# Optimization experiments

Measured on AMD Instinct MI355X. Metric: run time of the kernel, lower is better.

Reference implementation:

```python
import jax, jax.numpy as jnp
import numpy as np

EPS = 1e-6
K = 20  # n_knn from init


def _vnt_weight(W):
    # VNT linear: rows normalized to sum to 1 (which_norm_VNT='norm') for translation equivariance
    return W / jnp.sum(W, axis=1, keepdims=True)


def _lin(W, x):
    # apply [out,in] weight over channel axis 1 of x: [B, C_in, 3, ...] -> [B, C_out, 3, ...]
    return jnp.einsum('oi,bi...->bo...', W, x)


def _vn_lrelu(x, Wf, Wd, vnt=False):
    # VN(T)LinearLeakyReLU with negative_slope=0.0, no batchnorm. Vector axis is axis 2.
    Wp = _vnt_weight(Wf) if vnt else Wf
    p = _lin(Wp, x)
    d = _lin(Wd, x)
    dot = jnp.sum(p * d, axis=2, keepdims=True)
    dsq = jnp.sum(d * d, axis=2, keepdims=True)
    return jnp.where(dot >= 0, p, p - (dot / (dsq + EPS)) * d)


def _knn(pts, k):
    # pts: [B,N,3] -> indices of k nearest (self included), via -||xi-xj||^2 top_k
    sq = jnp.sum(pts * pts, axis=-1)                      # [B,N]
    inner = jnp.einsum('bnd,bmd->bnm', pts, pts)          # [B,N,N]
    neg_dist = 2.0 * inner - sq[:, :, None] - sq[:, None, :]
    return jax.lax.top_k(neg_dist, k)[1]                  # [B,N,k]


def _graph_feature_cross(x, k):
    # x: [B,3,N] -> edge features [B, 3(feat: nbr-ctr, ctr, cross), 3(vec), N, k]
    pts = jnp.transpose(x, (0, 2, 1))                     # [B,N,3]
    idx = _knn(pts, k)                                    # [B,N,k]
    nbr = jax.vmap(lambda p, i: p[i])(pts, idx)           # [B,N,k,3]
    ctr = jnp.broadcast_to(pts[:, :, None, :], nbr.shape)
    cross = jnp.cross(nbr, ctr)
    feat = jnp.stack([nbr - ctr, ctr, cross], axis=3)     # [B,N,k,3feat,3vec]
    return jnp.transpose(feat, (0, 3, 4, 1, 2))           # [B,3feat,3vec,N,k]


def _forward(x, Wpos_f, Wpos_d, Wc1_f, Wc1_d, Wc2_f, Wc2_d, Wt_f, Wt_d, W1_f, W1_d, W2_f, W2_d, W3):
    feat = _graph_feature_cross(x, K)                     # [B,3,3,N,K]
    h = _vn_lrelu(feat, Wpos_f, Wpos_d, vnt=True)         # [B,64,3,N,K]
    h = h.mean(axis=-1)                                   # mean pool over k -> [B,64,3,N]
    x2 = _vn_lrelu(h, Wc1_f, Wc1_d, vnt=True)             # conv_center_
    xc = _vn_lrelu(x2, Wc2_f, Wc2_d, vnt=True)            # conv_center
    tx = _vn_lrelu(xc, Wt_f, Wt_d, vnt=True)              # conv_trans [B,12,3,N]
    trans_latent = tx.mean(axis=-1)                       # [B,12,3]
    h = h - xc                                            # center features
    h = _vn_lrelu(h, W1_f, W1_d)                          # conv1
    h = _vn_lrelu(h, W2_f, W2_d)                          # conv2
    h = _lin(W3, h)                                       # conv3 (plain VNLinear) [B,116,3,N]
    rot_latent = h.mean(axis=-1)                          # [B,116,3]
    return jnp.concatenate([rot_latent, trans_latent], axis=1)  # [B,128,3]


def setup_inputs() -> dict:
    key = jax.random.key(0)
    ks = jax.random.split(key, 16)
    B, N, C = 4, 4096, 64
    ROT = 116  # c_dim - trans_c_dim

    def w(k, o, i):
        return jax.random.normal(k, (o, i), jnp.float32) * 0.1

    def wt(k, o, i):
        # VNT weights: row sums kept near 1 so normalization is well-conditioned
        return jax.random.normal(k, (o, i), jnp.float32) * 0.02 + 1.0 / i

    return {
        'x': jax.random.normal(ks[0], (B, 3, N), jnp.float32),
        'Wpos_f': wt(ks[1], C, 3), 'Wpos_d': w(ks[2], C, 3),
        'Wc1_f': wt(ks[3], C, C), 'Wc1_d': w(ks[4], C, C),
        'Wc2_f': wt(ks[5], C, C), 'Wc2_d': w(ks[6], C, C),
        'Wt_f': wt(ks[7], 12, C), 'Wt_d': w(ks[8], 12, C),
        'W1_f': w(ks[9], C, C), 'W1_d': w(ks[10], C, C),
        'W2_f': w(ks[11], C, C), 'W2_d': w(ks[12], C, C),
        'W3': w(ks[13], ROT, C),
    }


def reference(x, Wpos_f, Wpos_d, Wc1_f, Wc1_d, Wc2_f, Wc2_d, Wt_f, Wt_d, W1_f, W1_d, W2_f, W2_d, W3):
    return _forward(x, Wpos_f, Wpos_d, Wc1_f, Wc1_d, Wc2_f, Wc2_d, Wt_f, Wt_d, W1_f, W1_d, W2_f, W2_d, W3)
```

## Files before the change

### kernel.cpp

```cpp
#include <hip/hip_runtime.h>

#define NPTS 4096
#define BATCH 4
#define KNN 20
#define ROT 116

__device__ __forceinline__ void vn_lrelu3(float p[3], const float d[3]) {
  float dot = p[0]*d[0] + p[1]*d[1] + p[2]*d[2];
  if (dot < 0.0f) {
    float dsq = d[0]*d[0] + d[1]*d[1] + d[2]*d[2];
    float r = dot / (dsq + 1e-6f);
    p[0] -= r*d[0]; p[1] -= r*d[1]; p[2] -= r*d[2];
  }
}

__global__ __launch_bounds__(256) void knn_edge_kernel(const float* __restrict__ x,
                                                       const float* __restrict__ Wf,
                                                       const float* __restrict__ Wd,
                                                       float* __restrict__ h) {
  const int row = blockIdx.x;
  const int b = row >> 12, i = row & (NPTS - 1);
  const float* __restrict__ xb = x + b * 3 * NPTS;
  const float cx = xb[i], cy = xb[NPTS + i], cz = xb[2 * NPTS + i];
  const int t = threadIdx.x;
  const int j0 = t << 4;

  __shared__ unsigned int hist[2048];
  __shared__ unsigned int ld_[384];
  __shared__ int lj_[384];
  __shared__ unsigned int lcount;
  __shared__ int s_B;
  __shared__ int wtot[4];
  __shared__ int s_nbr[KNN];
  __shared__ float e[KNN][3][3];
  __shared__ float part[4][64][3];

  for (int k = t; k < 2048; k += 256) hist[k] = 0u;
  if (t == 0) lcount = 0u;
  __syncthreads();

  unsigned int db[16];
#pragma unroll
  for (int q = 0; q < 4; ++q) {
    const float4 px = *(const float4*)(xb + j0 + 4 * q);
    const float4 py = *(const float4*)(xb + NPTS + j0 + 4 * q);
    const float4 pz = *(const float4*)(xb + 2 * NPTS + j0 + 4 * q);
    float dx, dy, dz, dd;
    dx = px.x - cx; dy = py.x - cy; dz = pz.x - cz;
    dd = dx*dx + dy*dy + dz*dz; db[4*q+0] = __float_as_uint(dd);
    dx = px.y - cx; dy = py.y - cy; dz = pz.y - cz;
    dd = dx*dx + dy*dy + dz*dz; db[4*q+1] = __float_as_uint(dd);
    dx = px.z - cx; dy = py.z - cy; dz = pz.z - cz;
    dd = dx*dx + dy*dy + dz*dz; db[4*q+2] = __float_as_uint(dd);
    dx = px.w - cx; dy = py.w - cy; dz = pz.w - cz;
    dd = dx*dx + dy*dy + dz*dz; db[4*q+3] = __float_as_uint(dd);
  }
#pragma unroll
  for (int s = 0; s < 16; ++s) atomicAdd(&hist[db[s] >> 20], 1u);
  __syncthreads();

  int v = 0;
#pragma unroll
  for (int s = 0; s < 8; ++s) v += (int)hist[t * 8 + s];
  const int myps = v;
  const int lane = t & 63;
#pragma unroll
  for (int off = 1; off < 64; off <<= 1) {
    int n = __shfl_up(v, off);
    if (lane >= off) v += n;
  }
  if (lane == 63) wtot[t >> 6] = v;
  __syncthreads();
  int woff = 0;
#pragma unroll
  for (int w = 0; w < 4; ++w) if (w < (t >> 6)) woff += wtot[w];
  const int cum_in = v + woff;
  const int cum_ex = cum_in - myps;
  if (cum_ex < KNN && cum_in >= KNN) {
    int cum = cum_ex, B = t * 8;
    for (int s = 0; s < 8; ++s) {
      const int hh = (int)hist[t * 8 + s];
      if (cum + hh >= KNN) { B = t * 8 + s; break; }
      cum += hh;
    }
    s_B = B;
  }
  __syncthreads();
  const unsigned int Bb = (unsigned int)s_B;
#pragma unroll
  for (int s = 0; s < 16; ++s) {
    if ((db[s] >> 20) <= Bb) {
      unsigned int pos = atomicAdd(&lcount, 1u);
      if (pos < 384u) { ld_[pos] = db[s]; lj_[pos] = j0 + s; }
    }
  }
  __syncthreads();
  const int n = min((int)lcount, 384);
  for (int idx = t; idx < n; idx += 256) {
    const unsigned int kd = ld_[idx]; const int kj = lj_[idx];
    int rank = 0;
    for (int m = 0; m < n; ++m) {
      const unsigned int md = ld_[m];
      rank += (md < kd || (md == kd && lj_[m] < kj)) ? 1 : 0;
    }
    if (rank < KNN) s_nbr[rank] = kj;
  }
  __syncthreads();

  if (t < KNN) {
    const int j = s_nbr[t];
    const float nx = xb[j], ny = xb[NPTS + j], nz = xb[2 * NPTS + j];
    e[t][0][0] = nx - cx; e[t][0][1] = ny - cy; e[t][0][2] = nz - cz;
    e[t][1][0] = cx;      e[t][1][1] = cy;      e[t][1][2] = cz;
    e[t][2][0] = ny * cz - nz * cy;
    e[t][2][1] = nz * cx - nx * cz;
    e[t][2][2] = nx * cy - ny * cx;
  }
  __syncthreads();

  const int c = t & 63, kg = t >> 6;
  float f0 = Wf[c * 3 + 0], f1 = Wf[c * 3 + 1], f2 = Wf[c * 3 + 2];
  const float s = 1.0f / (f0 + f1 + f2);
  f0 *= s; f1 *= s; f2 *= s;
  const float d0 = Wd[c * 3 + 0], d1 = Wd[c * 3 + 1], d2 = Wd[c * 3 + 2];
  float a0 = 0.f, a1 = 0.f, a2 = 0.f;
#pragma unroll
  for (int kk = 0; kk < 5; ++kk) {
    const int k = kg * 5 + kk;
    float pv[3], dv[3];
#pragma unroll
    for (int vv = 0; vv < 3; ++vv) {
      pv[vv] = f0 * e[k][0][vv] + f1 * e[k][1][vv] + f2 * e[k][2][vv];
      dv[vv] = d0 * e[k][0][vv] + d1 * e[k][1][vv] + d2 * e[k][2][vv];
    }
    vn_lrelu3(pv, dv);
    a0 += pv[0]; a1 += pv[1]; a2 += pv[2];
  }
  part[kg][c][0] = a0; part[kg][c][1] = a1; part[kg][c][2] = a2;
  __syncthreads();
  if (t < 64) {
    const float inv = 1.0f / KNN;
    float* hp = h + (size_t)row * 192 + t * 3;
#pragma unroll
    for (int vv = 0; vv < 3; ++vv)
      hp[vv] = (part[0][t][vv] + part[1][t][vv] + part[2][t][vv] + part[3][t][vv]) * inv;
  }
}

template<bool VNT, int MODE>
__global__ __launch_bounds__(256) void layer_batch(
    const float* in, float* out, float* aux,
    const float* __restrict__ Wf, const float* __restrict__ Wd) {
  __shared__ float wfT[64][65], wdT[64][65];
  __shared__ float act[4][4][64][4];
  const int t = threadIdx.x, q = t >> 6, c = t & 63;
  for (int e = t; e < 4096; e += 256) {
    wfT[e & 63][e >> 6] = Wf[e];
    wdT[e & 63][e >> 6] = Wd[e];
  }
  __syncthreads();
  if (VNT) {
    if (t < 64) {
      float s = 0.f;
      for (int i = 0; i < 64; ++i) s += wfT[i][t];
      s = 1.0f / s;
      for (int i = 0; i < 64; ++i) wfT[i][t] *= s;
    }
    __syncthreads();
  }
  const int pbase = (blockIdx.x * 4 + q) * 8;
  float r0 = 0.f, r1 = 0.f, r2 = 0.f;
  for (int pass = 0; pass < 2; ++pass) {
    const int p0 = pbase + pass * 4;
#pragma unroll
    for (int p = 0; p < 4; ++p) {
      const float* ip = in + (size_t)(p0 + p) * 192 + c * 3;
      *(float4*)act[q][p][c] = make_float4(ip[0], ip[1], ip[2], 0.f);
    }
    __builtin_amdgcn_wave_barrier();
    float af[12], ad[12];
#pragma unroll
    for (int e = 0; e < 12; ++e) { af[e] = 0.f; ad[e] = 0.f; }
    for (int i = 0; i < 64; ++i) {
      const float wfv = wfT[i][c];
      const float wdv = wdT[i][c];
#pragma unroll
      for (int p = 0; p < 4; ++p) {
        const float4 hv = *(const float4*)act[q][p][i];
        af[p*3+0] += wfv * hv.x; af[p*3+1] += wfv * hv.y; af[p*3+2] += wfv * hv.z;
        ad[p*3+0] += wdv * hv.x; ad[p*3+1] += wdv * hv.y; ad[p*3+2] += wdv * hv.z;
      }
    }
    __builtin_amdgcn_wave_barrier();
#pragma unroll
    for (int p = 0; p < 4; ++p) {
      float pf[3] = { af[p*3+0], af[p*3+1], af[p*3+2] };
      float pd[3] = { ad[p*3+0], ad[p*3+1], ad[p*3+2] };
      vn_lrelu3(pf, pd);
      const size_t ofs = (size_t)(p0 + p) * 192 + c * 3;
      if (MODE == 0) {
        out[ofs+0] = pf[0]; out[ofs+1] = pf[1]; out[ofs+2] = pf[2];
      } else if (MODE == 1) {
        const float h0 = aux[ofs+0], h1 = aux[ofs+1], h2 = aux[ofs+2];
        aux[ofs+0] = h0 - pf[0]; aux[ofs+1] = h1 - pf[1]; aux[ofs+2] = h2 - pf[2];
        out[ofs+0] = pf[0]; out[ofs+1] = pf[1]; out[ofs+2] = pf[2];
      } else {
        r0 += pf[0]; r1 += pf[1]; r2 += pf[2];
      }
    }
    __builtin_amdgcn_wave_barrier();
  }
  if (MODE == 2) {
    *(float4*)act[q][0][c] = make_float4(r0, r1, r2, 0.f);
    __syncthreads();
    if (t < 192) {
      const int cc = t / 3, vv = t - cc * 3;
      out[blockIdx.x * 192 + t] =
          act[0][0][cc][vv] + act[1][0][cc][vv] + act[2][0][cc][vv] + act[3][0][cc][vv];
    }
  }
}

__global__ __launch_bounds__(256) void trans_kernel(
    const float* __restrict__ xc,
    const float* __restrict__ Wtf, const float* __restrict__ Wtd,
    float* __restrict__ trans_part) {
  __shared__ float wtf[12][65], wtd[12][65];
  __shared__ float xpt[4][64][4];
  __shared__ float tred[4][12][3];
  const int t = threadIdx.x, q = t >> 6, l = t & 63;
  for (int e = t; e < 768; e += 256) {
    wtf[e >> 6][e & 63] = Wtf[e]; wtd[e >> 6][e & 63] = Wtd[e];
  }
  __syncthreads();
  if (t < 12) {
    float s = 0.f;
    for (int i = 0; i < 64; ++i) s += wtf[t][i];
    s = 1.0f / s;
    for (int i = 0; i < 64; ++i) wtf[t][i] *= s;
  }
  __syncthreads();
  const int cch = l >> 2, v = l & 3;
  const bool act = (cch < 12) && (v < 3);
  float ta = 0.f;
  const int pbase = (blockIdx.x * 4 + q) * 8;
  for (int g = 0; g < 8; ++g) {
    const float* xp = xc + (size_t)(pbase + g) * 192 + l * 3;
    xpt[q][l][0] = xp[0]; xpt[q][l][1] = xp[1]; xpt[q][l][2] = xp[2];
    __builtin_amdgcn_wave_barrier();
    float pf = 0.f, pd = 0.f;
    if (act) {
      for (int i = 0; i < 64; ++i) {
        const float a = xpt[q][i][v];
        pf += wtf[cch][i] * a;
        pd += wtd[cch][i] * a;
      }
    }
    float pp = pf * pd, dd = pd * pd;
    pp += __shfl_xor(pp, 1); pp += __shfl_xor(pp, 2);
    dd += __shfl_xor(dd, 1); dd += __shfl_xor(dd, 2);
    if (pp < 0.f) pf -= (pp / (dd + 1e-6f)) * pd;
    ta += pf;
    __builtin_amdgcn_wave_barrier();
  }
  if (act) { tred[q][cch][v] = ta; }
  __syncthreads();
  if (t < 36) {
    const int cc = t / 3, vv = t - cc * 3;
    trans_part[blockIdx.x * 36 + t] =
        tred[0][cc][vv] + tred[1][cc][vv] + tred[2][cc][vv] + tred[3][cc][vv];
  }
}

__global__ __launch_bounds__(384) void finalize_kernel(const float* __restrict__ rot_part,
                                                       const float* __restrict__ trans_part,
                                                       const float* __restrict__ W3,
                                                       float* __restrict__ out) {
  const int b = blockIdx.x;
  const int t = threadIdx.x;
  __shared__ float hsum[64][3];
  if (t < 192) {
    float s = 0.f;
    for (int blk = 0; blk < 128; ++blk)
      s += rot_part[(b * 128 + blk) * 192 + t];
    hsum[t / 3][t % 3] = s * (1.0f / NPTS);
  } else if (t < 228) {
    const int tt = t - 192;
    float s = 0.f;
    for (int blk = 0; blk < 128; ++blk)
      s += trans_part[(b * 128 + blk) * 36 + tt];
    out[b * 384 + 348 + tt] = s * (1.0f / NPTS);
  }
  __syncthreads();
  if (t < 348) {
    const int ch = t / 3, v = t - ch * 3;
    float s = 0.f;
    for (int i = 0; i < 64; ++i) s += W3[ch * 64 + i] * hsum[i][v];
    out[b * 384 + t] = s;
  }
}

extern "C" void kernel_launch(void* const* d_in, const int* in_sizes, int n_in,
                              void* d_out, int out_size, void* d_ws, size_t ws_size,
                              hipStream_t stream) {
  (void)in_sizes; (void)n_in; (void)out_size; (void)ws_size;
  const float* x     = (const float*)d_in[0];
  const float* Wposf = (const float*)d_in[1];
  const float* Wposd = (const float*)d_in[2];
  const float* Wc1f  = (const float*)d_in[3];
  const float* Wc1d  = (const float*)d_in[4];
  const float* Wc2f  = (const float*)d_in[5];
  const float* Wc2d  = (const float*)d_in[6];
  const float* Wtf   = (const float*)d_in[7];
  const float* Wtd   = (const float*)d_in[8];
  const float* W1f   = (const float*)d_in[9];
  const float* W1d   = (const float*)d_in[10];
  const float* W2f   = (const float*)d_in[11];
  const float* W2d   = (const float*)d_in[12];
  const float* W3    = (const float*)d_in[13];
  float* out = (float*)d_out;

  char* ws = (char*)d_ws;
  float* P          = (float*)(ws + 1310720);
  float* Q          = (float*)(ws + 13893632);
  float* trans_part = (float*)(ws + 26476544);
  float* rot_part   = (float*)(ws + 26550272);

  knn_edge_kernel<<<BATCH * NPTS, 256, 0, stream>>>(x, Wposf, Wposd, P);
  layer_batch<true, 0><<<512, 256, 0, stream>>>(P, Q, nullptr, Wc1f, Wc1d);
  layer_batch<true, 1><<<512, 256, 0, stream>>>(Q, Q, P, Wc2f, Wc2d);
  trans_kernel<<<512, 256, 0, stream>>>(Q, Wtf, Wtd, trans_part);
  layer_batch<false, 0><<<512, 256, 0, stream>>>(P, P, nullptr, W1f, W1d);
  layer_batch<false, 2><<<512, 256, 0, stream>>>(P, rot_part, nullptr, W2f, W2d);
  finalize_kernel<<<BATCH, 384, 0, stream>>>(rot_part, trans_part, W3, out);
}
```

Measured before the change: 214.3 us.

## Process two query points per block in kNN edge kernel with packed histograms

Each block now handles two query rows, reusing the loaded point coordinates for both distance computations. The two histograms are packed into one shared array as low and high 16-bit halves, and the candidate counter is packed the same way, so the histogram, scan and threshold passes are shared. This halves the block count and amortises global loads, histogram clearing and the scan. In exchange there are more registers per thread, the ranking step runs on only 128 threads per row, and more shared memory is used, which may lower occupancy.

```diff
diff --git a/kernel.cpp b/kernel.cpp
--- a/kernel.cpp
+++ b/kernel.cpp
@@ -14,119 +14,179 @@
   }
 }
 
-__global__ __launch_bounds__(256) void knn_edge_kernel(const float* __restrict__ x,
-                                                       const float* __restrict__ Wf,
-                                                       const float* __restrict__ Wd,
-                                                       float* __restrict__ h) {
-  const int row = blockIdx.x;
-  const int b = row >> 12, i = row & (NPTS - 1);
+__global__ __launch_bounds__(256) void knn_edge2_kernel(const float* __restrict__ x,
+                                                        const float* __restrict__ Wf,
+                                                        const float* __restrict__ Wd,
+                                                        float* __restrict__ h) {
+  const int blk = blockIdx.x;
+  const int rowA = blk << 1, rowB = rowA + 1;
+  const int b = rowA >> 12;
+  const int iA = rowA & (NPTS - 1), iB = rowB & (NPTS - 1);
   const float* __restrict__ xb = x + b * 3 * NPTS;
-  const float cx = xb[i], cy = xb[NPTS + i], cz = xb[2 * NPTS + i];
+  const float cxA = xb[iA], cyA = xb[NPTS + iA], czA = xb[2 * NPTS + iA];
+  const float cxB = xb[iB], cyB = xb[NPTS + iB], czB = xb[2 * NPTS + iB];
   const int t = threadIdx.x;
   const int j0 = t << 4;
 
   __shared__ unsigned int hist[2048];
-  __shared__ unsigned int ld_[384];
-  __shared__ int lj_[384];
+  __shared__ unsigned int ldA_[384], ldB_[384];
+  __shared__ int ljA_[384], ljB_[384];
   __shared__ unsigned int lcount;
-  __shared__ int s_B;
-  __shared__ int wtot[4];
-  __shared__ int s_nbr[KNN];
-  __shared__ float e[KNN][3][3];
-  __shared__ float part[4][64][3];
+  __shared__ int s_BA, s_BB;
+  __shared__ unsigned int wtot[4];
+  __shared__ int s_nbrA[KNN], s_nbrB[KNN];
+  __shared__ float eA[KNN][3][3], eB[KNN][3][3];
+  __shared__ float partA[2][64][3], partB[2][64][3];
 
   for (int k = t; k < 2048; k += 256) hist[k] = 0u;
   if (t == 0) lcount = 0u;
   __syncthreads();
 
-  unsigned int db[16];
+  unsigned int dbA[16], dbB[16];
 #pragma unroll
   for (int q = 0; q < 4; ++q) {
     const float4 px = *(const float4*)(xb + j0 + 4 * q);
     const float4 py = *(const float4*)(xb + NPTS + j0 + 4 * q);
     const float4 pz = *(const float4*)(xb + 2 * NPTS + j0 + 4 * q);
     float dx, dy, dz, dd;
-    dx = px.x - cx; dy = py.x - cy; dz = pz.x - cz;
-    dd = dx*dx + dy*dy + dz*dz; db[4*q+0] = __float_as_uint(dd);
-    dx = px.y - cx; dy = py.y - cy; dz = pz.y - cz;
-    dd = dx*dx + dy*dy + dz*dz; db[4*q+1] = __float_as_uint(dd);
-    dx = px.z - cx; dy = py.z - cy; dz = pz.z - cz;
-    dd = dx*dx + dy*dy + dz*dz; db[4*q+2] = __float_as_uint(dd);
-    dx = px.w - cx; dy = py.w - cy; dz = pz.w - cz;
-    dd = dx*dx + dy*dy + dz*dz; db[4*q+3] = __float_as_uint(dd);
-  }
-#pragma unroll
-  for (int s = 0; s < 16; ++s) atomicAdd(&hist[db[s] >> 20], 1u);
-  __syncthreads();
-
-  int v = 0;
-#pragma unroll
-  for (int s = 0; s < 8; ++s) v += (int)hist[t * 8 + s];
-  const int myps = v;
+    dx = px.x - cxA; dy = py.x - cyA; dz = pz.x - czA;
+    dd = dx*dx + dy*dy + dz*dz; dbA[4*q+0] = __float_as_uint(dd);
+    dx = px.y - cxA; dy = py.y - cyA; dz = pz.y - czA;
+    dd = dx*dx + dy*dy + dz*dz; dbA[4*q+1] = __float_as_uint(dd);
+    dx = px.z - cxA; dy = py.z - cyA; dz = pz.z - czA;
+    dd = dx*dx + dy*dy + dz*dz; dbA[4*q+2] = __float_as_uint(dd);
+    dx = px.w - cxA; dy = py.w - cyA; dz = pz.w - czA;
+    dd = dx*dx + dy*dy + dz*dz; dbA[4*q+3] = __float_as_uint(dd);
+    dx = px.x - cxB; dy = py.x - cyB; dz = pz.x - czB;
+    dd = dx*dx + dy*dy + dz*dz; dbB[4*q+0] = __float_as_uint(dd);
+    dx = px.y - cxB; dy = py.y - cyB; dz = pz.y - czB;
+    dd = dx*dx + dy*dy + dz*dz; dbB[4*q+1] = __float_as_uint(dd);
+    dx = px.z - cxB; dy = py.z - cyB; dz = pz.z - czB;
+    dd = dx*dx + dy*dy + dz*dz; dbB[4*q+2] = __float_as_uint(dd);
+    dx = px.w - cxB; dy = py.w - cyB; dz = pz.w - czB;
+    dd = dx*dx + dy*dy + dz*dz; dbB[4*q+3] = __float_as_uint(dd);
+  }
+#pragma unroll
+  for (int s = 0; s < 16; ++s) {
+    atomicAdd(&hist[dbA[s] >> 20], 1u);
+    atomicAdd(&hist[dbB[s] >> 20], 0x10000u);
+  }
+  __syncthreads();
+
+  unsigned int v = 0;
+#pragma unroll
+  for (int s = 0; s < 8; ++s) v += hist[t * 8 + s];
+  const unsigned int myps = v;
   const int lane = t & 63;
 #pragma unroll
   for (int off = 1; off < 64; off <<= 1) {
-    int n = __shfl_up(v, off);
+    unsigned int n = (unsigned int)__shfl_up((int)v, off);
     if (lane >= off) v += n;
   }
   if (lane == 63) wtot[t >> 6] = v;
   __syncthreads();
-  int woff = 0;
+  unsigned int woff = 0;
 #pragma unroll
   for (int w = 0; w < 4; ++w) if (w < (t >> 6)) woff += wtot[w];
-  const int cum_in = v + woff;
-  const int cum_ex = cum_in - myps;
-  if (cum_ex < KNN && cum_in >= KNN) {
-    int cum = cum_ex, B = t * 8;
-    for (int s = 0; s < 8; ++s) {
-      const int hh = (int)hist[t * 8 + s];
-      if (cum + hh >= KNN) { B = t * 8 + s; break; }
-      cum += hh;
-    }
-    s_B = B;
-  }
-  __syncthreads();
-  const unsigned int Bb = (unsigned int)s_B;
+  const unsigned int cum_in = v + woff;
+  const unsigned int cum_ex = cum_in - myps;
+  {
+    const int ci = (int)(cum_in & 0xffffu), ce = (int)(cum_ex & 0xffffu);
+    if (ce < KNN && ci >= KNN) {
+      int cum = ce, B = t * 8;
+      for (int s = 0; s < 8; ++s) {
+        const int hh = (int)(hist[t * 8 + s] & 0xffffu);
+        if (cum + hh >= KNN) { B = t * 8 + s; break; }
+        cum += hh;
+      }
+      s_BA = B;
+    }
+  }
+  {
+    const int ci = (int)(cum_in >> 16), ce = (int)(cum_ex >> 16);
+    if (ce < KNN && ci >= KNN) {
+      int cum = ce, B = t * 8;
+      for (int s = 0; s < 8; ++s) {
+        const int hh = (int)(hist[t * 8 + s] >> 16);
+        if (cum + hh >= KNN) { B = t * 8 + s; break; }
+        cum += hh;
+      }
+      s_BB = B;
+    }
+  }
+  __syncthreads();
+  const unsigned int BA = (unsigned int)s_BA, BB = (unsigned int)s_BB;
 #pragma unroll
   for (int s = 0; s < 16; ++s) {
-    if ((db[s] >> 20) <= Bb) {
-      unsigned int pos = atomicAdd(&lcount, 1u);
-      if (pos < 384u) { ld_[pos] = db[s]; lj_[pos] = j0 + s; }
-    }
-  }
-  __syncthreads();
-  const int n = min((int)lcount, 384);
-  for (int idx = t; idx < n; idx += 256) {
-    const unsigned int kd = ld_[idx]; const int kj = lj_[idx];
-    int rank = 0;
-    for (int m = 0; m < n; ++m) {
-      const unsigned int md = ld_[m];
-      rank += (md < kd || (md == kd && lj_[m] < kj)) ? 1 : 0;
-    }
-    if (rank < KNN) s_nbr[rank] = kj;
+    if ((dbA[s] >> 20) <= BA) {
+      unsigned int old = atomicAdd(&lcount, 1u);
+      unsigned int pos = old & 0xffffu;
+      if (pos < 384u) { ldA_[pos] = dbA[s]; ljA_[pos] = j0 + s; }
+    }
+    if ((dbB[s] >> 20) <= BB) {
+      unsigned int old = atomicAdd(&lcount, 0x10000u);
+      unsigned int pos = old >> 16;
+      if (pos < 384u) { ldB_[pos] = dbB[s]; ljB_[pos] = j0 + s; }
+    }
+  }
+  __syncthreads();
+  const int nA = min((int)(lcount & 0xffffu), 384);
+  const int nB = min((int)(lcount >> 16), 384);
+  if (t < 128) {
+    for (int idx = t; idx < nA; idx += 128) {
+      const unsigned int kd = ldA_[idx]; const int kj = ljA_[idx];
+      int rank = 0;
+      for (int m = 0; m < nA; ++m) {
+        const unsigned int md = ldA_[m];
+        rank += (md < kd || (md == kd && ljA_[m] < kj)) ? 1 : 0;
+      }
+      if (rank < KNN) s_nbrA[rank] = kj;
+    }
+  } else {
+    for (int idx = t - 128; idx < nB; idx += 128) {
+      const unsigned int kd = ldB_[idx]; const int kj = ljB_[idx];
+      int rank = 0;
+      for (int m = 0; m < nB; ++m) {
+        const unsigned int md = ldB_[m];
+        rank += (md < kd || (md == kd && ljB_[m] < kj)) ? 1 : 0;
+      }
+      if (rank < KNN) s_nbrB[rank] = kj;
+    }
   }
   __syncthreads();
 
   if (t < KNN) {
-    const int j = s_nbr[t];
+    const int j = s_nbrA[t];
     const float nx = xb[j], ny = xb[NPTS + j], nz = xb[2 * NPTS + j];
-    e[t][0][0] = nx - cx; e[t][0][1] = ny - cy; e[t][0][2] = nz - cz;
-    e[t][1][0] = cx;      e[t][1][1] = cy;      e[t][1][2] = cz;
-    e[t][2][0] = ny * cz - nz * cy;
-    e[t][2][1] = nz * cx - nx * cz;
-    e[t][2][2] = nx * cy - ny * cx;
-  }
-  __syncthreads();
-
-  const int c = t & 63, kg = t >> 6;
+    eA[t][0][0] = nx - cxA; eA[t][0][1] = ny - cyA; eA[t][0][2] = nz - czA;
+    eA[t][1][0] = cxA;      eA[t][1][1] = cyA;      eA[t][1][2] = czA;
+    eA[t][2][0] = ny * czA - nz * cyA;
+    eA[t][2][1] = nz * cxA - nx * czA;
+    eA[t][2][2] = nx * cyA - ny * cxA;
+  } else if (t >= 64 && t < 64 + KNN) {
+    const int k = t - 64;
+    const int j = s_nbrB[k];
+    const float nx = xb[j], ny = xb[NPTS + j], nz = xb[2 * NPTS + j];
+    eB[k][0][0] = nx - cxB; eB[k][0][1] = ny - cyB; eB[k][0][2] = nz - czB;
+    eB[k][1][0] = cxB;      eB[k][1][1] = cyB;      eB[k][1][2] = czB;
+    eB[k][2][0] = ny * czB - nz * cyB;
+    eB[k][2][1] = nz * cxB - nx * czB;
+    eB[k][2][2] = nx * cyB - ny * cxB;
+  }
+  __syncthreads();
+
+  const int c = t & 63;
+  const int half = t >> 7;
+  const int kg = (t >> 6) & 1;
   float f0 = Wf[c * 3 + 0], f1 = Wf[c * 3 + 1], f2 = Wf[c * 3 + 2];
   const float s = 1.0f / (f0 + f1 + f2);
   f0 *= s; f1 *= s; f2 *= s;
   const float d0 = Wd[c * 3 + 0], d1 = Wd[c * 3 + 1], d2 = Wd[c * 3 + 2];
   float a0 = 0.f, a1 = 0.f, a2 = 0.f;
-#pragma unroll
-  for (int kk = 0; kk < 5; ++kk) {
-    const int k = kg * 5 + kk;
+  const float (*e)[3][3] = (half == 0) ? eA : eB;
+#pragma unroll
+  for (int kk = 0; kk < 10; ++kk) {
+    const int k = kg * 10 + kk;
     float pv[3], dv[3];
 #pragma unroll
     for (int vv = 0; vv < 3; ++vv) {
@@ -136,14 +196,22 @@
     vn_lrelu3(pv, dv);
     a0 += pv[0]; a1 += pv[1]; a2 += pv[2];
   }
-  part[kg][c][0] = a0; part[kg][c][1] = a1; part[kg][c][2] = a2;
+  if (half == 0) { partA[kg][c][0] = a0; partA[kg][c][1] = a1; partA[kg][c][2] = a2; }
+  else           { partB[kg][c][0] = a0; partB[kg][c][1] = a1; partB[kg][c][2] = a2; }
   __syncthreads();
   if (t < 64) {
     const float inv = 1.0f / KNN;
-    float* hp = h + (size_t)row * 192 + t * 3;
+    float* hp = h + (size_t)rowA * 192 + t * 3;
 #pragma unroll
     for (int vv = 0; vv < 3; ++vv)
-      hp[vv] = (part[0][t][vv] + part[1][t][vv] + part[2][t][vv] + part[3][t][vv]) * inv;
+      hp[vv] = (partA[0][t][vv] + partA[1][t][vv]) * inv;
+  } else if (t < 128) {
+    const int cc = t - 64;
+    const float inv = 1.0f / KNN;
+    float* hp = h + (size_t)rowB * 192 + cc * 3;
+#pragma unroll
+    for (int vv = 0; vv < 3; ++vv)
+      hp[vv] = (partB[0][cc][vv] + partB[1][cc][vv]) * inv;
   }
 }
 
@@ -326,7 +394,7 @@
   float* trans_part = (float*)(ws + 26476544);
   float* rot_part   = (float*)(ws + 26550272);
 
-  knn_edge_kernel<<<BATCH * NPTS, 256, 0, stream>>>(x, Wposf, Wposd, P);
+  knn_edge2_kernel<<<BATCH * NPTS / 2, 256, 0, stream>>>(x, Wposf, Wposd, P);
   layer_batch<true, 0><<<512, 256, 0, stream>>>(P, Q, nullptr, Wc1f, Wc1d);
   layer_batch<true, 1><<<512, 256, 0, stream>>>(Q, Q, P, Wc2f, Wc2d);
   trans_kernel<<<512, 256, 0, stream>>>(Q, Wtf, Wtd, trans_part);
```

Measured after the change: 204.7 us. 4.5% less time.
